# Kernel tuning notes

Measured on AMD Instinct MI355X. Metric: run time of the kernel, lower is better.

Reference implementation:

```python
import jax, jax.numpy as jnp
import numpy as np

EPS = 1e-5  # torch BatchNorm1d default eps


def _bn(x, axes):
    # BatchNorm in training mode with gamma=1, beta=0 (torch init values):
    # normalize with biased batch statistics over the given axes.
    m = x.mean(axes, keepdims=True)
    v = x.var(axes, keepdims=True)
    return (x - m) * jax.lax.rsqrt(v + EPS)


def setup_inputs() -> dict:
    key = jax.random.key(0)
    ks = jax.random.split(key, 12)
    N, M = 50000, 12
    OF, F, E, H = 92, 64, 41, 128
    Z = 2 * F + E  # 169 = concat(node, nbr_node, edge)

    def w(k, shape, fan):
        return jax.random.normal(k, shape, jnp.float32) * np.float32(1.0 / np.sqrt(fan))

    return {
        "node_fea": jax.random.normal(ks[0], (N, OF), jnp.float32),
        "edge_fea": jax.random.uniform(ks[1], (N, M, E), dtype=jnp.float32),
        "nbr_offset": jax.random.randint(ks[2], (N, M, 3), -1, 2).astype(jnp.float32),
        "atom_pos": jax.random.uniform(ks[3], (N, 3), dtype=jnp.float32) * 10.0,
        "cells": jnp.broadcast_to(jnp.eye(3, dtype=jnp.float32) * 10.0, (N, 3, 3))
                 + jax.random.normal(ks[4], (N, 3, 3), jnp.float32) * 0.1,
        "edge_idx": jax.random.randint(ks[5], (N, M), 0, N),
        "W_emb": w(ks[6], (OF, F), OF), "b_emb": jnp.zeros((F,), jnp.float32),
        "W_pre_node": w(ks[7], (3, Z, 2 * F), Z), "b_pre_node": jnp.zeros((3, 2 * F), jnp.float32),
        "W_pre_edge": w(ks[8], (3, Z, 2 * E), Z), "b_pre_edge": jnp.zeros((3, 2 * E), jnp.float32),
        "W_dist": w(ks[9], (Z, H), Z), "b_dist": jnp.zeros((H,), jnp.float32),
        "W_const": w(ks[10], (Z, H), Z), "b_const": jnp.zeros((H,), jnp.float32),
    }


def reference(node_fea, edge_fea, nbr_offset, atom_pos, cells, edge_idx,
              W_emb, b_emb, W_pre_node, b_pre_node, W_pre_edge, b_pre_edge,
              W_dist, b_dist, W_const, b_const):
    N, M = edge_idx.shape
    lrelu = jax.nn.leaky_relu  # torch LeakyReLU default slope 0.01
    sig = jax.nn.sigmoid
    sp = jax.nn.softplus

    # get_distance: neighbor Cartesian positions via unit-cell offsets
    off_cart = jnp.einsum('nmi,nij->nmj', nbr_offset, cells)         # (N,M,3)
    diff = atom_pos[edge_idx] + off_cart - atom_pos[:, None, :]       # (N,M,3)
    distance = jnp.sqrt(jnp.sum(diff * diff, -1, keepdims=True) + 1e-12)  # (N,M,1)

    node = node_fea @ W_emb + b_emb  # embedding -> (N,64)

    for l in range(W_pre_node.shape[0]):  # n_conv = 3 ConvLayers
        nbr = node[edge_idx]  # gather (N,M,F)
        z = jnp.concatenate(
            [jnp.broadcast_to(node[:, None, :], (N, M, node.shape[-1])), nbr, edge_fea],
            axis=2)  # (N,M,169)
        # node branch: linear -> BN -> sigmoid*leakyrelu gate -> sum over M -> BN -> residual
        zn = _bn(z @ W_pre_node[l] + b_pre_node[l], (0, 1))  # (N,M,128)
        nf, nc = jnp.split(zn, 2, axis=2)
        aggr = jnp.sum(sig(nf) * lrelu(nc), axis=1)           # (N,64)
        node = lrelu(node + _bn(aggr, (0,)))
        # edge branch: linear -> BN -> gate -> BN -> residual
        ze = _bn(z @ W_pre_edge[l] + b_pre_edge[l], (0, 1))   # (N,M,82)
        ef, ec = jnp.split(ze, 2, axis=2)
        edge_fea = lrelu(edge_fea + _bn(sig(ef) * lrelu(ec), (0, 1)))

    nbr = node[edge_idx]
    bond_fea = jnp.concatenate(
        [jnp.broadcast_to(node[:, None, :], (N, M, node.shape[-1])), nbr, edge_fea],
        axis=2)  # (N,M,169)

    # n_h_dist == 1 branch: softplus(BN(linear) + distance), mean over channels
    bd = sp(_bn(bond_fea @ W_dist + b_dist, (0, 1)) + distance)
    bd = jnp.mean(bd, axis=2, keepdims=True)                  # (N,M,1)
    # n_h_const == 1 branch: softplus(BN(linear)), mean over channels, / N
    bc = sp(_bn(bond_fea @ W_const + b_const, (0, 1)))
    bc = jnp.mean(bc, axis=2, keepdims=True) / N              # (N,M,1)

    return jnp.concatenate([bd, bc], axis=2)                  # (N,M,2)
```

## Files before the change

### kernel.cpp

```cpp
#include <hip/hip_runtime.h>
#include <math.h>

#define NN 50000
#define MM 12
#define NM 600000
#define OF 92
#define FF 64
#define EE 41
#define ES 48
#define ZZ 169
#define RPB 96
#define NPB 8
#define NTILE 6250
#define KSTEPS 6
#define MT 6
#define NSLICE 64
#define PSTRIDE 1024
#define TPB 512
#define Z1OFF 0
#define Z2OFF 13824
#define Z0OFF 27648
#define SMEMB 28800

typedef __bf16 bf16x8 __attribute__((ext_vector_type(8)));
typedef float  f32x4  __attribute__((ext_vector_type(4)));

__device__ __forceinline__ float lrelu(float x){ return fmaxf(x, 0.01f*x); }
__device__ __forceinline__ float sigm(float x){ return __builtin_amdgcn_rcpf(1.f+__expf(-x)); }
__device__ __forceinline__ float softpl(float x){ return fmaxf(x,0.f) + __logf(1.f+__expf(-fabsf(x))); }
__device__ __forceinline__ unsigned short f2bf(float f){
    __bf16 h = (__bf16)f;
    return __builtin_bit_cast(unsigned short, h);
}
__device__ __forceinline__ float b2f(unsigned short u){
    unsigned int b = ((unsigned int)u) << 16;
    return __builtin_bit_cast(float, b);
}

__global__ __launch_bounds__(256) void pack_w(const float* __restrict__ Wn,
    const float* __restrict__ We, const float* __restrict__ Wd,
    const float* __restrict__ Wc, unsigned short* __restrict__ dst)
{
    int idx = blockIdx.x*256 + threadIdx.x;
    if (idx >= 4*49152) return;
    int j    = idx & 7;
    int lane = (idx >> 3) & 63;
    int ntks = (idx >> 9) % 96;
    int L    = idx / 49152;
    int nt = ntks & 15, ks = ntks >> 4;
    int k   = ks*32 + (lane>>4)*8 + j;
    int col = nt*16 + (lane&15);
    float v = 0.f;
    if (k < ZZ) {
        if (L < 3) {
            if (col < 128)                       v = Wn[((size_t)L*ZZ + k)*128 + col];
            else if (col >= 128 && col < 128+EE) v = We[((size_t)L*ZZ + k)*82 + (col-128)];
            else if (col >= 192 && col < 192+EE) v = We[((size_t)L*ZZ + k)*82 + 41 + (col-192)];
        } else {
            if (col < 128) v = Wd[(size_t)k*128 + col];
            else           v = Wc[(size_t)k*128 + (col-128)];
        }
    }
    dst[idx] = f2bf(v);
}

__global__ __launch_bounds__(256) void k_dist(const float* __restrict__ off,
    const float* __restrict__ apos, const float* __restrict__ cells,
    const int* __restrict__ eidx, float* __restrict__ distb)
{
    int idx = blockIdx.x*256 + threadIdx.x;
    if (idx >= NM) return;
    int n = idx / MM;
    const float* o  = off + (size_t)idx*3;
    const float* cl = cells + (size_t)n*9;
    int n2 = eidx[idx];
    float o0=o[0], o1=o[1], o2=o[2];
    float dd = 1e-12f;
    #pragma unroll
    for (int j=0;j<3;j++){
        float oc = o0*cl[0*3+j] + o1*cl[1*3+j] + o2*cl[2*3+j];
        float d = apos[(size_t)n2*3+j] + oc - apos[(size_t)n*3+j];
        dd += d*d;
    }
    distb[idx] = sqrtf(dd);
}

__global__ __launch_bounds__(256) void k_cvt(const float* __restrict__ src,
    unsigned short* __restrict__ e)
{
    int idx = blockIdx.x*256 + threadIdx.x;
    if (idx >= NM*6) return;
    int gr = idx / 6;
    int ch = idx - gr*6;
    const float* s = src + (size_t)gr*EE + ch*8;
    unsigned short os[8];
    #pragma unroll
    for (int j=0;j<8;j++){
        int c = ch*8+j;
        os[j] = (c < EE) ? f2bf(s[j]) : (unsigned short)0;
    }
    *(uint4*)(e + (size_t)gr*ES + ch*8) = *(uint4*)os;
}

__global__ __launch_bounds__(256) void k_emb(const float* __restrict__ nf,
    const float* __restrict__ W, const float* __restrict__ b,
    unsigned short* __restrict__ node0)
{
    int idx = blockIdx.x*256 + threadIdx.x;
    if (idx >= NN*FF) return;
    int n = idx >> 6, c = idx & 63;
    float s = b[c];
    for (int k=0;k<OF;k++) s = fmaf(nf[(size_t)n*OF+k], W[k*FF+c], s);
    node0[idx] = f2bf(s);
}

__global__ __launch_bounds__(256) void k_red(float* __restrict__ P,
    float* __restrict__ dst, int lo, int hi)
{
    for (int c = lo + threadIdx.x; c < hi; c += 256) {
        float s = 0.f;
        #pragma unroll 8
        for (int sl = 0; sl < NSLICE; ++sl) s += P[sl*PSTRIDE + c];
        dst[c] = s;
        #pragma unroll 8
        for (int sl = 0; sl < NSLICE; ++sl) P[sl*PSTRIDE + c] = 0.f;
    }
}

__device__ __forceinline__ uint4 upd_edge8(uint4 e, uint4 g,
    const float* __restrict__ mmv, const float* __restrict__ isv, int ch)
{
    unsigned short es[8], gs[8], os[8];
    *(uint4*)es = e; *(uint4*)gs = g;
    #pragma unroll
    for (int j=0;j<8;j++){
        int c = ch*8+j;
        if (c < EE){
            float v = (b2f(gs[j]) - mmv[j]) * isv[j];
            os[j] = f2bf(lrelu(b2f(es[j]) + v));
        } else os[j] = es[j];
    }
    return *(uint4*)os;
}

template<bool UPD>
__device__ __forceinline__ void stage_z(char* smem,
    const unsigned short* __restrict__ node_src, unsigned short* __restrict__ ebuf,
    const unsigned short* __restrict__ gbuf, const int* __restrict__ eidx,
    int n0, int tid, const float* __restrict__ mmv, const float* __restrict__ isv)
{
    unsigned short* Z1 = (unsigned short*)(smem + Z1OFF);
    unsigned short* Z2 = (unsigned short*)(smem + Z2OFF);
    unsigned short* Z0 = (unsigned short*)(smem + Z0OFF);
    const int gr0 = n0 * MM;
    const int r0 = tid >> 3, ch = tid & 7;
    const bool two = tid < 256;
    const int r1 = r0 + 64;
    int e0 = eidx[gr0 + r0];
    uint4 nb0 = *(const uint4*)(node_src + (size_t)e0*FF + ch*8);
    *(uint4*)(Z1 + r0*72 + ch*8) = nb0;
    if (two) {
        int e1 = eidx[gr0 + r1];
        uint4 nb1 = *(const uint4*)(node_src + (size_t)e1*FF + ch*8);
        *(uint4*)(Z1 + r1*72 + ch*8) = nb1;
    }
    {
        uint4 v = make_uint4(0u,0u,0u,0u);
        if (ch < 6) {
            v = *(const uint4*)(ebuf + (size_t)(gr0+r0)*ES + ch*8);
            if (UPD) {
                uint4 g = *(const uint4*)(gbuf + (size_t)(gr0+r0)*ES + ch*8);
                v = upd_edge8(v, g, mmv, isv, ch);
                *(uint4*)(ebuf + (size_t)(gr0+r0)*ES + ch*8) = v;
            }
        }
        *(uint4*)(Z2 + r0*72 + ch*8) = v;
        if (two) {
            uint4 v1 = make_uint4(0u,0u,0u,0u);
            if (ch < 6) {
                v1 = *(const uint4*)(ebuf + (size_t)(gr0+r1)*ES + ch*8);
                if (UPD) {
                    uint4 g1 = *(const uint4*)(gbuf + (size_t)(gr0+r1)*ES + ch*8);
                    v1 = upd_edge8(v1, g1, mmv, isv, ch);
                    *(uint4*)(ebuf + (size_t)(gr0+r1)*ES + ch*8) = v1;
                }
            }
            *(uint4*)(Z2 + r1*72 + ch*8) = v1;
        }
    }
    if (tid >= 448) {
        int nd = (tid - 448) >> 3;
        uint4 s = *(const uint4*)(node_src + (size_t)(n0+nd)*FF + ch*8);
        *(uint4*)(Z0 + nd*72 + ch*8) = s;
    }
}

__device__ __forceinline__ void mfma_core(const char* smem,
    const unsigned short* __restrict__ Wpk, int h, int sw, int lane, f32x4 (&acc)[MT][2])
{
    const int quad = lane >> 4, li = lane & 15;
    const unsigned short* Z1 = (const unsigned short*)(smem + Z1OFF);
    const unsigned short* Z2 = (const unsigned short*)(smem + Z2OFF);
    const unsigned short* Z0 = (const unsigned short*)(smem + Z0OFF);
    #pragma unroll
    for (int mt=0;mt<MT;mt++){
        acc[mt][0] = (f32x4){0.f,0.f,0.f,0.f};
        acc[mt][1] = (f32x4){0.f,0.f,0.f,0.f};
    }
    int rd12[MT];
    #pragma unroll
    for (int mt=0;mt<MT;mt++) rd12[mt] = ((mt*16 + li) * 2731) >> 15;
    const int nt0 = h*8 + sw;
    #pragma unroll
    for (int ks=0; ks<KSTEPS; ++ks) {
        bf16x8 bfr0 = *(const bf16x8*)(Wpk + (((ks*16 + nt0    )*64 + lane) << 3));
        bf16x8 bfr1 = *(const bf16x8*)(Wpk + (((ks*16 + nt0 + 4)*64 + lane) << 3));
        bf16x8 afr[MT];
        #pragma unroll
        for (int mt=0;mt<MT;mt++){
            int row = mt*16 + li;
            if (ks < 2)
                afr[mt] = *(const bf16x8*)(Z0 + rd12[mt]*72 + ks*32 + quad*8);
            else if (ks < 4)
                afr[mt] = *(const bf16x8*)(Z1 + row*72 + (ks-2)*32 + quad*8);
            else
                afr[mt] = *(const bf16x8*)(Z2 + row*72 + (ks-4)*32 + quad*8);
        }
        #pragma unroll
        for (int mt=0;mt<MT;mt++){
            acc[mt][0] = __builtin_amdgcn_mfma_f32_16x16x32_bf16(afr[mt], bfr0, acc[mt][0], 0, 0, 0);
            acc[mt][1] = __builtin_amdgcn_mfma_f32_16x16x32_bf16(afr[mt], bfr1, acc[mt][1], 0, 0, 0);
        }
    }
}

__device__ __forceinline__ void stats_epi(const f32x4 (&acc)[MT][2], int h, int sw, int lane,
    float* __restrict__ Ps)
{
    const int quad = lane>>4, li = lane&15;
    #pragma unroll
    for (int t=0;t<2;t++){
        float s=0.f, q=0.f;
        #pragma unroll
        for (int mt=0;mt<MT;mt++)
            #pragma unroll
            for (int r=0;r<4;r++){ float v = acc[mt][t][r]; s+=v; q = fmaf(v,v,q); }
        s += __shfl_xor(s,16); s += __shfl_xor(s,32);
        q += __shfl_xor(q,16); q += __shfl_xor(q,32);
        if (quad == 0) {
            int col = h*128 + t*64 + sw*16 + li;
            atomicAdd(&Ps[col], s);
            atomicAdd(&Ps[256+col], q);
        }
    }
}

template<bool UPD>
__device__ __forceinline__ void k_stats_body(
    const unsigned short* __restrict__ node_src, unsigned short* __restrict__ ebuf,
    const unsigned short* __restrict__ gbuf, const int* __restrict__ eidx,
    const unsigned short* __restrict__ Wpk,
    const float* __restrict__ gS, const float* __restrict__ gQ,
    float* __restrict__ Pst)
{
    __shared__ __align__(16) char smem[SMEMB];
    const int tid = threadIdx.x, w = tid>>6, lane = tid&63;
    const int h = w>>2, sw = w&3;
    const int ch = tid & 7;
    float mmv[8], isv[8];
    if (UPD) {
        #pragma unroll
        for (int j=0;j<8;j++){
            int c = ch*8+j;
            float mm = 0.f, is = 0.f;
            if (c < EE) {
                mm = gS[c]*(1.f/(float)NM);
                float vv = gQ[c]*(1.f/(float)NM) - mm*mm;
                is = rsqrtf(vv + 1e-5f);
            }
            mmv[j] = mm; isv[j] = is;
        }
    }
    const int n0 = blockIdx.x * NPB;
    stage_z<UPD>(smem, node_src, ebuf, gbuf, eidx, n0, tid, mmv, isv);
    __syncthreads();
    f32x4 acc[MT][2];
    mfma_core(smem, Wpk, h, sw, lane, acc);
    float* Ps = Pst + (size_t)(blockIdx.x & (NSLICE-1))*PSTRIDE;
    stats_epi(acc, h, sw, lane, Ps);
}

__global__ __launch_bounds__(TPB,3) void k_stats0(
    const unsigned short* __restrict__ node_src, unsigned short* __restrict__ ebuf,
    const int* __restrict__ eidx, const unsigned short* __restrict__ Wpk,
    float* __restrict__ Pst)
{
    k_stats_body<false>(node_src, ebuf, nullptr, eidx, Wpk, nullptr, nullptr, Pst);
}

__global__ __launch_bounds__(TPB,3) void k_stats_u(
    const unsigned short* __restrict__ node_src, unsigned short* __restrict__ ebuf,
    const unsigned short* __restrict__ gbuf, const int* __restrict__ eidx,
    const unsigned short* __restrict__ Wpk,
    const float* __restrict__ gS, const float* __restrict__ gQ,
    float* __restrict__ Pst)
{
    k_stats_body<true>(node_src, ebuf, gbuf, eidx, Wpk, gS, gQ, Pst);
}

__global__ __launch_bounds__(TPB,3) void k_apply_re(
    const unsigned short* __restrict__ node_src, unsigned short* __restrict__ ebuf,
    const int* __restrict__ eidx, const unsigned short* __restrict__ Wpk,
    const float* __restrict__ preS, const float* __restrict__ preQ,
    float* __restrict__ aggr, unsigned short* __restrict__ gbuf,
    float* __restrict__ Pst)
{
    __shared__ __align__(16) char smem[SMEMB];
    float* gL = (float*)smem;
    const int tid = threadIdx.x, w = tid>>6, lane = tid&63;
    const int quad = lane>>4, li = lane&15;
    const int h = w>>2, sw = w&3;
    const int n0 = blockIdx.x * NPB;
    const int gr0 = n0 * MM;
    stage_z<false>(smem, node_src, ebuf, nullptr, eidx, n0, tid, nullptr, nullptr);
    __syncthreads();
    f32x4 acc[MT][2];
    mfma_core(smem, Wpk, h, sw, lane, acc);
    __syncthreads();

    const int cg0 = sw*16 + li;
    float sc[2], bi[2];
    #pragma unroll
    for (int t=0;t<2;t++){
        int col = h*128 + t*64 + cg0;
        float mm = preS[col]*(1.f/(float)NM);
        float vv = preQ[col]*(1.f/(float)NM) - mm*mm;
        float is = rsqrtf(vv + 1e-5f);
        sc[t] = is; bi[t] = -mm*is;
    }
    const bool ce_ok = cg0 < EE;
    float* Ps = Pst + (size_t)(blockIdx.x & (NSLICE-1))*PSTRIDE;

    if (h == 0) {
        #pragma unroll
        for (int mt=0;mt<MT;mt++)
            #pragma unroll
            for (int r=0;r<4;r++){
                int row = mt*16 + quad*4 + r;
                float nf = fmaf(acc[mt][0][r], sc[0], bi[0]);
                float nc = fmaf(acc[mt][1][r], sc[1], bi[1]);
                gL[row*68 + cg0] = sigm(nf) * lrelu(nc);
            }
    } else {
        float pg = 0.f, pq = 0.f;
        #pragma unroll
        for (int mt=0;mt<MT;mt++)
            #pragma unroll
            for (int r=0;r<4;r++){
                int row = mt*16 + quad*4 + r;
                float ef = fmaf(acc[mt][0][r], sc[0], bi[0]);
                float ec = fmaf(acc[mt][1][r], sc[1], bi[1]);
                float gv = sigm(ef)*lrelu(ec);
                if (ce_ok) {
                    gbuf[(size_t)(gr0+row)*ES + cg0] = f2bf(gv);
                    pg += gv; pq = fmaf(gv,gv,pq);
                }
            }
        pg += __shfl_xor(pg,16); pg += __shfl_xor(pg,32);
        pq += __shfl_xor(pq,16); pq += __shfl_xor(pq,32);
        if (quad==0 && ce_ok){ atomicAdd(&Ps[640+cg0], pg); atomicAdd(&Ps[704+cg0], pq); }
    }
    __syncthreads();
    {
        float vsum = 0.f;
        #pragma unroll
        for (int jj=0;jj<MM;jj++) vsum += gL[(w*MM+jj)*68 + lane];
        aggr[(size_t)(n0+w)*64 + lane] = vsum;
        atomicAdd(&Ps[512+lane], vsum);
        atomicAdd(&Ps[576+lane], vsum*vsum);
    }
}

__global__ __launch_bounds__(256) void k_upd_node(const unsigned short* __restrict__ cur,
    const float* __restrict__ aggr, const float* __restrict__ aS,
    const float* __restrict__ aQ, unsigned short* __restrict__ nxt)
{
    int idx = blockIdx.x*256 + threadIdx.x;
    if (idx >= NN*8) return;
    int n = idx >> 3, ch = idx & 7;
    int base = n*64 + ch*8;
    float4 a0 = *(const float4*)(aggr + base);
    float4 a1 = *(const float4*)(aggr + base + 4);
    uint4 cu = *(const uint4*)(cur + base);
    unsigned short cs[8]; *(uint4*)cs = cu;
    float av[8] = {a0.x,a0.y,a0.z,a0.w,a1.x,a1.y,a1.z,a1.w};
    unsigned short os[8];
    #pragma unroll
    for (int j=0;j<8;j++){
        int c = ch*8+j;
        float mm = aS[c]*(1.f/(float)NN);
        float vv = aQ[c]*(1.f/(float)NN) - mm*mm;
        float is = rsqrtf(vv + 1e-5f);
        float v = (av[j] - mm) * is;
        os[j] = f2bf(lrelu(b2f(cs[j]) + v));
    }
    *(uint4*)(nxt + base) = *(uint4*)os;
}

__global__ __launch_bounds__(TPB,3) void k_final_re(
    const unsigned short* __restrict__ node_src, unsigned short* __restrict__ ebuf,
    const int* __restrict__ eidx, const unsigned short* __restrict__ Wpk,
    const float* __restrict__ fS, const float* __restrict__ fQ,
    const float* __restrict__ distb, float* __restrict__ out)
{
    __shared__ __align__(16) char smem[SMEMB];
    float* bufD = (float*)smem;
    float* bufC = (float*)(smem + 8192);
    const int tid = threadIdx.x, w = tid>>6, lane = tid&63;
    const int quad = lane>>4, li = lane&15;
    const int h = w>>2, sw = w&3;
    const int n0 = blockIdx.x * NPB;
    const int gr0 = n0 * MM;
    stage_z<false>(smem, node_src, ebuf, nullptr, eidx, n0, tid, nullptr, nullptr);
    __syncthreads();
    f32x4 acc[MT][2];
    mfma_core(smem, Wpk, h, sw, lane, acc);
    __syncthreads();

    const int cg0 = sw*16 + li;
    float sc[2], bi[2];
    #pragma unroll
    for (int t=0;t<2;t++){
        int col = h*128 + t*64 + cg0;
        float mm = fS[col]*(1.f/(float)NM);
        float vv = fQ[col]*(1.f/(float)NM) - mm*mm;
        float is = rsqrtf(vv + 1e-5f);
        sc[t] = is; bi[t] = -mm*is;
    }
    const int liq = li >> 2;
    const bool wr = (li & 3) == 0;
    float* buf = (h == 0) ? bufD : bufC;
    #pragma unroll
    for (int mt=0;mt<MT;mt++)
        #pragma unroll
        for (int r=0;r<4;r++){
            int row = mt*16 + quad*4 + r;
            float v0 = fmaf(acc[mt][0][r], sc[0], bi[0]);
            float v1 = fmaf(acc[mt][1][r], sc[1], bi[1]);
            float p;
            if (h == 0) {
                float dv = distb[gr0 + row];
                p = softpl(v0 + dv) + softpl(v1 + dv);
            } else {
                p = softpl(v0) + softpl(v1);
            }
            p += __shfl_xor(p,1); p += __shfl_xor(p,2);
            if (wr) buf[row*17 + sw*4 + liq] = p;
        }
    __syncthreads();
    if (tid < 2*RPB) {
        int hh = tid >= RPB;
        int row = tid - (hh ? RPB : 0);
        const float* bsrc = hh ? bufC : bufD;
        float s = 0.f;
        #pragma unroll
        for (int t=0;t<16;t++) s += bsrc[row*17+t];
        size_t gr = gr0 + row;
        out[gr*2 + hh] = hh ? s * (1.f/128.f) * (1.f/(float)NN) : s * (1.f/128.f);
    }
}

extern "C" void kernel_launch(void* const* d_in, const int* in_sizes, int n_in,
                              void* d_out, int out_size, void* d_ws, size_t ws_size,
                              hipStream_t stream)
{
    const float* node_fea = (const float*)d_in[0];
    const float* edge_in  = (const float*)d_in[1];
    const float* nbr_off  = (const float*)d_in[2];
    const float* apos     = (const float*)d_in[3];
    const float* cells    = (const float*)d_in[4];
    const int*   eidx     = (const int*)  d_in[5];
    const float* W_emb    = (const float*)d_in[6];
    const float* b_emb    = (const float*)d_in[7];
    const float* W_pn     = (const float*)d_in[8];
    const float* W_pe     = (const float*)d_in[10];
    const float* W_dist   = (const float*)d_in[12];
    const float* W_cst    = (const float*)d_in[14];
    float* out = (float*)d_out;
    char* ws = (char*)d_ws;

    size_t o = 0;
    auto alloc = [&](size_t bytes) { char* p = ws + o; o += (bytes + 255) & ~(size_t)255; return p; };
    unsigned short* node0 = (unsigned short*)alloc((size_t)NN*FF*2);
    unsigned short* node1 = (unsigned short*)alloc((size_t)NN*FF*2);
    unsigned short* ebuf  = (unsigned short*)alloc((size_t)NM*ES*2);
    unsigned short* gbuf  = (unsigned short*)alloc((size_t)NM*ES*2);
    float* aggr  = (float*)alloc((size_t)NN*FF*4);
    float* distb = (float*)alloc((size_t)NM*4);
    unsigned short* Wpk = (unsigned short*)alloc((size_t)4*49152*2);
    float* stats = (float*)alloc(4096*4);
    float* Pst   = (float*)alloc((size_t)NSLICE*PSTRIDE*4);

    hipMemsetAsync(stats, 0, 4096*sizeof(float), stream);
    hipMemsetAsync(Pst, 0, (size_t)NSLICE*PSTRIDE*sizeof(float), stream);
    pack_w<<<(4*49152+255)/256, 256, 0, stream>>>(W_pn, W_pe, W_dist, W_cst, Wpk);
    k_dist <<<(NM+255)/256,     256, 0, stream>>>(nbr_off, apos, cells, eidx, distb);
    k_cvt  <<<(NM*6+255)/256,   256, 0, stream>>>(edge_in, ebuf);
    k_emb  <<<(NN*FF+255)/256,  256, 0, stream>>>(node_fea, W_emb, b_emb, node0);

    const unsigned short* ncur = node0;

    for (int l=0;l<3;l++){
        float* st = stats + l*768;
        float* preS = st;       float* preQ = st+256;
        float* aSs  = st+512;   float* aQq  = st+576;
        const unsigned short* Wl = Wpk + (size_t)l*49152;
        unsigned short* ndst = (l & 1) ? node0 : node1;

        if (l == 0) {
            k_stats0 <<<NTILE,TPB,0,stream>>>((const unsigned short*)ncur, ebuf, eidx, Wl, Pst);
        } else {
            const float* gSp = stats + (l-1)*768 + 640;
            const float* gQp = stats + (l-1)*768 + 704;
            k_stats_u<<<NTILE,TPB,0,stream>>>((const unsigned short*)ncur, ebuf, gbuf, eidx,
                                              Wl, gSp, gQp, Pst);
        }
        k_red    <<<1,256,0,stream>>>(Pst, st, 0, 512);
        k_apply_re<<<NTILE,TPB,0,stream>>>((const unsigned short*)ncur, ebuf, eidx, Wl,
                                           preS, preQ, aggr, gbuf, Pst);
        k_red    <<<1,256,0,stream>>>(Pst, st, 512, 768);
        k_upd_node<<<(NN*8+255)/256,256,0,stream>>>(ncur, aggr, aSs, aQq, ndst);
        ncur = ndst;
    }

    float* fSt = stats + 3*768;
    float* fS = fSt; float* fQ = fSt + 256;
    const unsigned short* Wf = Wpk + (size_t)3*49152;
    const float* gSp = stats + 2*768 + 640;
    const float* gQp = stats + 2*768 + 704;
    k_stats_u<<<NTILE,TPB,0,stream>>>((const unsigned short*)ncur, ebuf, gbuf, eidx,
                                      Wf, gSp, gQp, Pst);
    k_red    <<<1,256,0,stream>>>(Pst, fSt, 0, 512);
    k_final_re<<<NTILE,TPB,0,stream>>>((const unsigned short*)ncur, ebuf, eidx, Wf,
                                       fS, fQ, distb, out);
}
```

Baseline: 1.191 ms.

## Tile embedding GEMV in shared memory; use separate LDS buffers to drop post-MFMA barriers

The embedding kernel now stages the weight matrix and a 32-node tile of input features in shared memory, and each thread computes 8 output channels with vectorized weight reads and a 16-byte store. This replaces one-thread-per-output with strided global reads. In the apply and final kernels, the scratch buffers previously aliased onto the staging smem get their own shared arrays, so the __syncthreads after the MFMA core can be removed. The cost is extra LDS per block, which may reduce occupancy under the launch bounds of 3 blocks per CU.

```diff
diff --git a/kernel.cpp b/kernel.cpp
--- a/kernel.cpp
+++ b/kernel.cpp
@@ -106,12 +106,40 @@
     const float* __restrict__ W, const float* __restrict__ b,
     unsigned short* __restrict__ node0)
 {
-    int idx = blockIdx.x*256 + threadIdx.x;
-    if (idx >= NN*FF) return;
-    int n = idx >> 6, c = idx & 63;
-    float s = b[c];
-    for (int k=0;k<OF;k++) s = fmaf(nf[(size_t)n*OF+k], W[k*FF+c], s);
-    node0[idx] = f2bf(s);
+    __shared__ float Wl[OF*FF];
+    __shared__ float bl[FF];
+    __shared__ float nfl[32*OF];
+    const int tid = threadIdx.x;
+    const int n0 = blockIdx.x * 32;
+    for (int i = tid; i < (OF*FF)/4; i += 256)
+        ((float4*)Wl)[i] = ((const float4*)W)[i];
+    if (tid < FF) bl[tid] = b[tid];
+    {
+        const int lim4 = (min(32, NN - n0) * OF) / 4;
+        const float4* src4 = (const float4*)(nf + (size_t)n0*OF);
+        for (int i = tid; i < lim4; i += 256)
+            ((float4*)nfl)[i] = src4[i];
+    }
+    __syncthreads();
+    const int nl = tid >> 3;
+    const int c0 = (tid & 7) * 8;
+    if (n0 + nl >= NN) return;
+    float acc[8];
+    #pragma unroll
+    for (int j=0;j<8;j++) acc[j] = bl[c0+j];
+    for (int k=0;k<OF;k++){
+        float x = nfl[nl*OF + k];
+        const float4 w0 = *(const float4*)(Wl + k*FF + c0);
+        const float4 w1 = *(const float4*)(Wl + k*FF + c0 + 4);
+        acc[0] = fmaf(x, w0.x, acc[0]); acc[1] = fmaf(x, w0.y, acc[1]);
+        acc[2] = fmaf(x, w0.z, acc[2]); acc[3] = fmaf(x, w0.w, acc[3]);
+        acc[4] = fmaf(x, w1.x, acc[4]); acc[5] = fmaf(x, w1.y, acc[5]);
+        acc[6] = fmaf(x, w1.z, acc[6]); acc[7] = fmaf(x, w1.w, acc[7]);
+    }
+    unsigned short os[8];
+    #pragma unroll
+    for (int j=0;j<8;j++) os[j] = f2bf(acc[j]);
+    *(uint4*)(node0 + (size_t)(n0+nl)*FF + c0) = *(uint4*)os;
 }
 
 __global__ __launch_bounds__(256) void k_red(float* __restrict__ P,
@@ -316,7 +344,7 @@
     float* __restrict__ Pst)
 {
     __shared__ __align__(16) char smem[SMEMB];
-    float* gL = (float*)smem;
+    __shared__ float gL[RPB*68];
     const int tid = threadIdx.x, w = tid>>6, lane = tid&63;
     const int quad = lane>>4, li = lane&15;
     const int h = w>>2, sw = w&3;
@@ -326,7 +354,6 @@
     __syncthreads();
     f32x4 acc[MT][2];
     mfma_core(smem, Wpk, h, sw, lane, acc);
-    __syncthreads();
 
     const int cg0 = sw*16 + li;
     float sc[2], bi[2];
@@ -414,8 +441,8 @@
     const float* __restrict__ distb, float* __restrict__ out)
 {
     __shared__ __align__(16) char smem[SMEMB];
-    float* bufD = (float*)smem;
-    float* bufC = (float*)(smem + 8192);
+    __shared__ float bufD[RPB*17];
+    __shared__ float bufC[RPB*17];
     const int tid = threadIdx.x, w = tid>>6, lane = tid&63;
     const int quad = lane>>4, li = lane&15;
     const int h = w>>2, sw = w&3;
@@ -425,7 +452,6 @@
     __syncthreads();
     f32x4 acc[MT][2];
     mfma_core(smem, Wpk, h, sw, lane, acc);
-    __syncthreads();
 
     const int cg0 = sw*16 + li;
     float sc[2], bi[2];
@@ -506,7 +532,7 @@
     pack_w<<<(4*49152+255)/256, 256, 0, stream>>>(W_pn, W_pe, W_dist, W_cst, Wpk);
     k_dist <<<(NM+255)/256,     256, 0, stream>>>(nbr_off, apos, cells, eidx, distb);
     k_cvt  <<<(NM*6+255)/256,   256, 0, stream>>>(edge_in, ebuf);
-    k_emb  <<<(NN*FF+255)/256,  256, 0, stream>>>(node_fea, W_emb, b_emb, node0);
+    k_emb  <<<(NN+31)/32,       256, 0, stream>>>(node_fea, W_emb, b_emb, node0);
 
     const unsigned short* ncur = node0;
 
```

Result: faster. 1.157 ms (-2.9%).
